# Kernel tuning notes

Measured on AMD Instinct MI355X. Metric: run time of the kernel, lower is better.

Reference implementation:

```python
import jax, jax.numpy as jnp
import numpy as np

D, H, DH, FF, L = 1024, 8, 128, 2048, 3
TEXT_V, UNIT_V = 128257, 10001
LN_EPS = 1e-5
TEMP = 0.0005
NEG = -1e9


def _layer_norm(x, s, b):
    m = x.mean(-1, keepdims=True)
    v = ((x - m) ** 2).mean(-1, keepdims=True)
    return (x - m) / jnp.sqrt(v + LN_EPS) * s + b


def _encoder(tokens, pad_idx, emb, ipw, ipb, ow, ob, l1s, l1b, f1w, f1b, f2w, f2b, l2s, l2b):
    pad = tokens == pad_idx  # [B,S] key padding mask
    x = emb[tokens]  # [B,S,D]; padding row of emb is zero
    B, S, _ = x.shape
    scale = 1.0 / np.sqrt(DH).astype(np.float32)
    for l in range(L):
        # --- self attention (post-norm, PyTorch TransformerEncoderLayer default) ---
        qkv = x @ ipw[l].T + ipb[l]  # [B,S,3D]
        q, k, v = jnp.split(qkv, 3, axis=-1)
        q = q.reshape(B, S, H, DH)
        k = k.reshape(B, S, H, DH)
        v = v.reshape(B, S, H, DH)
        scores = jnp.einsum('bqhd,bkhd->bhqk', q, k) * scale
        scores = jnp.where(pad[:, None, None, :], NEG, scores)
        attn = jax.nn.softmax(scores, axis=-1)
        o = jnp.einsum('bhqk,bkhd->bqhd', attn, v).reshape(B, S, D)
        o = o @ ow[l].T + ob[l]
        x = _layer_norm(x + o, l1s[l], l1b[l])
        # --- feedforward ---
        ff = jax.nn.relu(x @ f1w[l].T + f1b[l]) @ f2w[l].T + f2b[l]
        x = _layer_norm(x + ff, l2s[l], l2b[l])
    return x, pad


def _enc_params(key, V):
    ks = jax.random.split(key, 4)
    emb = jax.random.normal(ks[0], (V, D), jnp.float32) * 0.02
    emb = emb.at[V - 1].set(0.0)  # padding_idx row is zero
    return dict(
        emb=emb,
        ipw=jax.random.normal(ks[1], (L, 3 * D, D), jnp.float32) * 0.02,
        ipb=jnp.zeros((L, 3 * D), jnp.float32),
        ow=jax.random.normal(ks[2], (L, D, D), jnp.float32) * 0.02,
        ob=jnp.zeros((L, D), jnp.float32),
        l1s=jnp.ones((L, D), jnp.float32),
        l1b=jnp.zeros((L, D), jnp.float32),
        f1w=jax.random.normal(ks[3], (L, FF, D), jnp.float32) * 0.02,
        f1b=jnp.zeros((L, FF), jnp.float32),
        f2w=jax.random.normal(jax.random.fold_in(ks[3], 1), (L, D, FF), jnp.float32) * 0.02,
        f2b=jnp.zeros((L, D), jnp.float32),
        l2s=jnp.ones((L, D), jnp.float32),
        l2b=jnp.zeros((L, D), jnp.float32),
    )


def setup_inputs() -> dict:
    key = jax.random.key(0)
    k_tt, k_ut, k_tp, k_up = jax.random.split(key, 4)
    B, T, U = 8, 256, 1024
    inp = {
        'text_tokens': jax.random.randint(k_tt, (B, T), 0, TEXT_V - 1, jnp.int32),
        'unit_tokens': jax.random.randint(k_ut, (B, U), 0, UNIT_V - 1, jnp.int32),
    }
    for name, p in _enc_params(k_tp, TEXT_V).items():
        inp['t_' + name] = p
    for name, p in _enc_params(k_up, UNIT_V).items():
        inp['u_' + name] = p
    return inp


def reference(text_tokens, unit_tokens,
              t_emb, t_ipw, t_ipb, t_ow, t_ob, t_l1s, t_l1b, t_f1w, t_f1b, t_f2w, t_f2b, t_l2s, t_l2b,
              u_emb, u_ipw, u_ipb, u_ow, u_ob, u_l1s, u_l1b, u_f1w, u_f1b, u_f2w, u_f2b, u_l2s, u_l2b):
    tf, tpad = _encoder(text_tokens, TEXT_V - 1, t_emb, t_ipw, t_ipb, t_ow, t_ob,
                        t_l1s, t_l1b, t_f1w, t_f1b, t_f2w, t_f2b, t_l2s, t_l2b)
    uf, upad = _encoder(unit_tokens, UNIT_V - 1, u_emb, u_ipw, u_ipb, u_ow, u_ob,
                        u_l1s, u_l1b, u_f1w, u_f1b, u_f2w, u_f2b, u_l2s, u_l2b)
    # squared L2 distance via |a-b|^2 = |a|^2 + |b|^2 - 2 a.b (avoids [B,U,T,D] tensor)
    un = jnp.sum(uf * uf, axis=-1)  # [B,U]
    tn = jnp.sum(tf * tf, axis=-1)  # [B,T]
    cross = jnp.einsum('bud,btd->but', uf, tf)  # [B,U,T]
    dist = -TEMP * (un[:, :, None] + tn[:, None, :] - 2.0 * cross)
    mask = upad[:, :, None] | tpad[:, None, :]
    filled = jnp.where(mask, NEG, dist)
    return jax.nn.log_softmax(filled, axis=-1)  # [B,U,T]
```

## Files before the change

kernel.cpp:

```cpp
#include <hip/hip_runtime.h>
#include <stdint.h>

typedef _Float16 half_t;
typedef _Float16 half8 __attribute__((ext_vector_type(8)));
typedef float floatx4 __attribute__((ext_vector_type(4)));

#define D_MODEL 1024
#define NHEAD 8
#define DHEAD 128
#define FF_DIM 2048
#define NLAYER 3
#define BATCH 8
#define TSEQ 256
#define USEQ 1024
#define TPAD 128256
#define UPAD 10000
#define TEMP_ 5e-4f
#define SCALE_QK 0.08838834764831845f

__device__ inline float blk_sum(float v, float* sh) {
#pragma unroll
  for (int o = 32; o; o >>= 1) v += __shfl_xor(v, o, 64);
  __syncthreads();
  if ((threadIdx.x & 63) == 0) sh[threadIdx.x >> 6] = v;
  __syncthreads();
  return sh[0] + sh[1] + sh[2] + sh[3];
}
__device__ inline float blk_max(float v, float* sh) {
#pragma unroll
  for (int o = 32; o; o >>= 1) v = fmaxf(v, __shfl_xor(v, o, 64));
  __syncthreads();
  if ((threadIdx.x & 63) == 0) sh[threadIdx.x >> 6] = v;
  __syncthreads();
  return fmaxf(fmaxf(sh[0], sh[1]), fmaxf(sh[2], sh[3]));
}

__global__ __launch_bounds__(256)
void gemm_bt_kernel(const half_t* __restrict__ A, long lda, long sAb, long sAz,
                    const half_t* __restrict__ B, long ldb, long sBb, long sBz,
                    float* __restrict__ Cf, half_t* __restrict__ Ch,
                    long ldc, long sCb, long sCz,
                    const float* __restrict__ bias,
                    int M, int N, int K, float alpha, int relu, int zdiv) {
  __shared__ __align__(16) half_t As[128 * 64];
  __shared__ __align__(16) half_t Bs[128 * 64];

  const int z = blockIdx.z;
  const int zb = z / zdiv, zh = z % zdiv;
  A += (long)zb * sAb + (long)zh * sAz;
  B += (long)zb * sBb + (long)zh * sBz;
  const long coff = (long)zb * sCb + (long)zh * sCz;

  const int tid = threadIdx.x;
  const int lane = tid & 63;
  const int wid = tid >> 6;
  const long row0 = (long)blockIdx.y * 128;
  const long col0 = (long)blockIdx.x * 128;

  const int srow = tid >> 3;
  const int sg = tid & 7;

  const int wm = (wid & 1) << 6;
  const int wn = (wid >> 1) << 6;
  const int fm = lane & 15;
  const int quad = lane >> 4;

  floatx4 acc[4][4] = {};

  for (int k0 = 0; k0 < K; k0 += 64) {
#pragma unroll
    for (int i = 0; i < 4; ++i) {
      const int r = srow + (i << 5);
      const int gsw = (sg ^ (r & 7)) << 3;
      uint4 va = *(const uint4*)(A + (row0 + r) * lda + k0 + (sg << 3));
      *(uint4*)(&As[(r << 6) + gsw]) = va;
      uint4 vb = *(const uint4*)(B + (col0 + r) * ldb + k0 + (sg << 3));
      *(uint4*)(&Bs[(r << 6) + gsw]) = vb;
    }
    __syncthreads();
#pragma unroll
    for (int kk = 0; kk < 64; kk += 32) {
      const int gq = (kk >> 3) + quad;
      half8 af[4], bfr[4];
#pragma unroll
      for (int mi = 0; mi < 4; ++mi) {
        const int r = wm + (mi << 4) + fm;
        af[mi] = *(const half8*)(&As[(r << 6) + ((gq ^ (r & 7)) << 3)]);
      }
#pragma unroll
      for (int ni = 0; ni < 4; ++ni) {
        const int r = wn + (ni << 4) + fm;
        bfr[ni] = *(const half8*)(&Bs[(r << 6) + ((gq ^ (r & 7)) << 3)]);
      }
#pragma unroll
      for (int mi = 0; mi < 4; ++mi)
#pragma unroll
        for (int ni = 0; ni < 4; ++ni)
          acc[mi][ni] = __builtin_amdgcn_mfma_f32_16x16x32_f16(af[mi], bfr[ni], acc[mi][ni], 0, 0, 0);
    }
    __syncthreads();
  }

#pragma unroll
  for (int ni = 0; ni < 4; ++ni) {
    const long col = col0 + wn + (ni << 4) + fm;
    const float bv = bias ? bias[col] : 0.0f;
#pragma unroll
    for (int mi = 0; mi < 4; ++mi) {
#pragma unroll
      for (int r = 0; r < 4; ++r) {
        const long row = row0 + wm + (mi << 4) + (quad << 2) + r;
        float v = acc[mi][ni][r] * alpha + bv;
        if (relu) v = fmaxf(v, 0.0f);
        const long idx = coff + row * ldc + col;
        if (Cf) Cf[idx] = v;
        if (Ch) Ch[idx] = (half_t)v;
      }
    }
  }
}

__global__ void cvt_kernel(const float* __restrict__ in, half_t* __restrict__ out, long n) {
  long i = (long)blockIdx.x * 256 + threadIdx.x;
  const long stride = (long)gridDim.x * 256;
  for (; i < n; i += stride) out[i] = (half_t)in[i];
}

__global__ __launch_bounds__(256) void embed_kernel(const int* __restrict__ tok,
                                                    const float* __restrict__ emb,
                                                    float* __restrict__ xf, half_t* __restrict__ xh) {
  const long r = blockIdx.x;
  const long src = (long)tok[r] * D_MODEL;
  for (int j = threadIdx.x; j < D_MODEL; j += 256) {
    const float v = emb[src + j];
    xf[r * D_MODEL + j] = v;
    xh[r * D_MODEL + j] = (half_t)v;
  }
}

__global__ __launch_bounds__(256) void ln_kernel(float* x, const float* y,
                                                 const float* s, const float* b, half_t* xh) {
  const int row = blockIdx.x, tid = threadIdx.x;
  float* xr = x + (long)row * D_MODEL;
  const float* yr = y + (long)row * D_MODEL;
  float v[4], sum = 0.f, sq = 0.f;
#pragma unroll
  for (int c = 0; c < 4; ++c) {
    const int j = tid + (c << 8);
    const float t = xr[j] + yr[j];
    v[c] = t; sum += t; sq += t * t;
  }
  __shared__ float sh[4];
  sum = blk_sum(sum, sh);
  sq = blk_sum(sq, sh);
  const float mean = sum * (1.0f / D_MODEL);
  const float var = sq * (1.0f / D_MODEL) - mean * mean;
  const float inv = rsqrtf(var + 1e-5f);
#pragma unroll
  for (int c = 0; c < 4; ++c) {
    const int j = tid + (c << 8);
    const float t = (v[c] - mean) * inv * s[j] + b[j];
    xr[j] = t;
    xh[(long)row * D_MODEL + j] = (half_t)t;
  }
}

__global__ __launch_bounds__(256) void softmax_kernel(half_t* sc, const int* __restrict__ tok,
                                                      int S, int padidx) {
  const int q = blockIdx.x, z = blockIdx.y;
  const int b = z >> 3;
  half_t* row = sc + (long)z * S * S + (long)q * S;
  const int* tb = tok + (long)b * S;
  const int nc = S >> 8;
  const int tid = threadIdx.x;
  float v[4];
  float m = -3e38f;
  for (int c = 0; c < nc; ++c) {
    const int j = tid + (c << 8);
    float x = (float)row[j];
    if (tb[j] == padidx) x = -1e9f;
    v[c] = x;
    m = fmaxf(m, x);
  }
  __shared__ float sh[4];
  m = blk_max(m, sh);
  float ssum = 0.f;
  for (int c = 0; c < nc; ++c) { v[c] = expf(v[c] - m); ssum += v[c]; }
  ssum = blk_sum(ssum, sh);
  const float inv = 1.0f / ssum;
  for (int c = 0; c < nc; ++c) row[tid + (c << 8)] = (half_t)(v[c] * inv);
}

__global__ __launch_bounds__(256) void vtrans_kernel(const half_t* __restrict__ qkv,
                                                     half_t* __restrict__ vt, int S) {
  __shared__ half_t tile[64][65];
  const int s0 = blockIdx.x * 64, d0 = blockIdx.y * 64, z = blockIdx.z;
  const int b = z >> 3, h = z & 7;
  const half_t* src = qkv + (long)b * S * (3 * D_MODEL) + 2 * D_MODEL + h * DHEAD;
  for (int idx = threadIdx.x; idx < 4096; idx += 256) {
    const int r = idx >> 6, c = idx & 63;
    tile[r][c] = src[(long)(s0 + r) * (3 * D_MODEL) + d0 + c];
  }
  __syncthreads();
  half_t* dst = vt + ((long)z * DHEAD + d0) * S + s0;
  for (int idx = threadIdx.x; idx < 4096; idx += 256) {
    const int r = idx >> 6, c = idx & 63;
    dst[(long)r * S + c] = tile[c][r];
  }
}

__global__ __launch_bounds__(256) void rowsq_kernel(const float* __restrict__ x, float* __restrict__ o) {
  const int row = blockIdx.x, tid = threadIdx.x;
  const float* xr = x + (long)row * D_MODEL;
  float s = 0.f;
#pragma unroll
  for (int c = 0; c < 4; ++c) { const float t = xr[tid + (c << 8)]; s += t * t; }
  __shared__ float sh[4];
  s = blk_sum(s, sh);
  if (tid == 0) o[row] = s;
}

__global__ __launch_bounds__(256) void dist_lsm_kernel(float* out, const float* __restrict__ un,
                                                       const float* __restrict__ tn,
                                                       const int* __restrict__ utok,
                                                       const int* __restrict__ ttok) {
  const int u = blockIdx.x, b = blockIdx.y, t = threadIdx.x;
  const long off = ((long)(b * USEQ + u)) * TSEQ;
  const float c = out[off + t];
  float x = -TEMP_ * (un[b * USEQ + u] + tn[b * TSEQ + t] - 2.0f * c);
  if (utok[b * USEQ + u] == UPAD || ttok[b * TSEQ + t] == TPAD) x = -1e9f;
  __shared__ float sh[4];
  const float m = blk_max(x, sh);
  const float e = expf(x - m);
  const float s = blk_sum(e, sh);
  out[off + t] = x - m - logf(s);
}

static void launch_gemm(hipStream_t st, const half_t* A, long lda, long sAb, long sAz,
                        const half_t* B, long ldb, long sBb, long sBz,
                        float* Cf, half_t* Ch, long ldc, long sCb, long sCz,
                        const float* bias, int M, int N, int K, float alpha, int relu,
                        int zdiv, int nz) {
  dim3 g(N / 128, M / 128, nz), blk(256);
  gemm_bt_kernel<<<g, blk, 0, st>>>(A, lda, sAb, sAz, B, ldb, sBb, sBz,
                                    Cf, Ch, ldc, sCb, sCz, bias, M, N, K, alpha, relu, zdiv);
}

struct EncW {
  const int* tok; int S;
  const float *emb, *ipb, *ob, *l1s, *l1b, *f1b, *f2b, *l2s, *l2b;
  const half_t *ipw, *ow, *f1w, *f2w;
  int padidx;
};
struct Bufs {
  float *xf, *yf;
  half_t *xh, *qkv, *vt, *sc, *oh, *ffh;
};

static void run_encoder(hipStream_t st, const EncW& w, const Bufs& bb) {
  const int S = w.S, Ntok = BATCH * S;
  embed_kernel<<<Ntok, 256, 0, st>>>(w.tok, w.emb, bb.xf, bb.xh);
  for (int l = 0; l < NLAYER; ++l) {
    launch_gemm(st, bb.xh, D_MODEL, 0, 0,
                w.ipw + (size_t)l * 3 * D_MODEL * D_MODEL, D_MODEL, 0, 0,
                nullptr, bb.qkv, 3 * D_MODEL, 0, 0,
                w.ipb + (size_t)l * 3 * D_MODEL, Ntok, 3 * D_MODEL, D_MODEL, 1.0f, 0, 1, 1);
    vtrans_kernel<<<dim3(S / 64, DHEAD / 64, BATCH * NHEAD), 256, 0, st>>>(bb.qkv, bb.vt, S);
    launch_gemm(st, bb.qkv, 3 * D_MODEL, (long)S * 3 * D_MODEL, DHEAD,
                bb.qkv + D_MODEL, 3 * D_MODEL, (long)S * 3 * D_MODEL, DHEAD,
                nullptr, bb.sc, S, (long)NHEAD * S * S, (long)S * S,
                nullptr, S, S, DHEAD, SCALE_QK, 0, NHEAD, BATCH * NHEAD);
    softmax_kernel<<<dim3(S, BATCH * NHEAD), 256, 0, st>>>(bb.sc, w.tok, S, w.padidx);
    launch_gemm(st, bb.sc, S, (long)NHEAD * S * S, (long)S * S,
                bb.vt, S, (long)NHEAD * DHEAD * S, (long)DHEAD * S,
                nullptr, bb.oh, D_MODEL, (long)S * D_MODEL, DHEAD,
                nullptr, S, DHEAD, S, 1.0f, 0, NHEAD, BATCH * NHEAD);
    launch_gemm(st, bb.oh, D_MODEL, 0, 0,
                w.ow + (size_t)l * D_MODEL * D_MODEL, D_MODEL, 0, 0,
                bb.yf, nullptr, D_MODEL, 0, 0,
                w.ob + (size_t)l * D_MODEL, Ntok, D_MODEL, D_MODEL, 1.0f, 0, 1, 1);
    ln_kernel<<<Ntok, 256, 0, st>>>(bb.xf, bb.yf, w.l1s + (size_t)l * D_MODEL,
                                    w.l1b + (size_t)l * D_MODEL, bb.xh);
    launch_gemm(st, bb.xh, D_MODEL, 0, 0,
                w.f1w + (size_t)l * FF_DIM * D_MODEL, D_MODEL, 0, 0,
                nullptr, bb.ffh, FF_DIM, 0, 0,
                w.f1b + (size_t)l * FF_DIM, Ntok, FF_DIM, D_MODEL, 1.0f, 1, 1, 1);
    launch_gemm(st, bb.ffh, FF_DIM, 0, 0,
                w.f2w + (size_t)l * D_MODEL * FF_DIM, FF_DIM, 0, 0,
                bb.yf, nullptr, D_MODEL, 0, 0,
                w.f2b + (size_t)l * D_MODEL, Ntok, D_MODEL, FF_DIM, 1.0f, 0, 1, 1);
    ln_kernel<<<Ntok, 256, 0, st>>>(bb.xf, bb.yf, w.l2s + (size_t)l * D_MODEL,
                                    w.l2b + (size_t)l * D_MODEL, bb.xh);
  }
}

extern "C" void kernel_launch(void* const* d_in, const int* in_sizes, int n_in,
                              void* d_out, int out_size, void* d_ws, size_t ws_size,
                              hipStream_t stream) {
  (void)in_sizes; (void)n_in; (void)out_size; (void)ws_size;
  const int* ttok = (const int*)d_in[0];
  const int* utok = (const int*)d_in[1];
  const float* tp[13];
  const float* up[13];
  for (int i = 0; i < 13; ++i) tp[i] = (const float*)d_in[2 + i];
  for (int i = 0; i < 13; ++i) up[i] = (const float*)d_in[15 + i];

  char* wp = (char*)d_ws;
  auto alloc = [&](size_t bytes) {
    void* p = wp;
    wp += (bytes + 255) & ~(size_t)255;
    return p;
  };
  const size_t IPW = (size_t)NLAYER * 3 * D_MODEL * D_MODEL;
  const size_t OW = (size_t)NLAYER * D_MODEL * D_MODEL;
  const size_t F1W = (size_t)NLAYER * FF_DIM * D_MODEL;
  const size_t F2W = (size_t)NLAYER * D_MODEL * FF_DIM;
  half_t* t_ipw = (half_t*)alloc(IPW * 2);
  half_t* t_ow = (half_t*)alloc(OW * 2);
  half_t* t_f1w = (half_t*)alloc(F1W * 2);
  half_t* t_f2w = (half_t*)alloc(F2W * 2);
  half_t* u_ipw = (half_t*)alloc(IPW * 2);
  half_t* u_ow = (half_t*)alloc(OW * 2);
  half_t* u_f1w = (half_t*)alloc(F1W * 2);
  half_t* u_f2w = (half_t*)alloc(F2W * 2);
  Bufs bb;
  bb.xf = (float*)alloc((size_t)BATCH * USEQ * D_MODEL * 4);
  bb.yf = (float*)alloc((size_t)BATCH * USEQ * D_MODEL * 4);
  bb.xh = (half_t*)alloc((size_t)BATCH * USEQ * D_MODEL * 2);
  bb.qkv = (half_t*)alloc((size_t)BATCH * USEQ * 3 * D_MODEL * 2);
  bb.vt = (half_t*)alloc((size_t)BATCH * NHEAD * DHEAD * USEQ * 2);
  bb.sc = (half_t*)alloc((size_t)BATCH * NHEAD * USEQ * USEQ * 2);
  bb.oh = (half_t*)alloc((size_t)BATCH * USEQ * D_MODEL * 2);
  bb.ffh = (half_t*)alloc((size_t)BATCH * USEQ * FF_DIM * 2);
  half_t* tfh = (half_t*)alloc((size_t)BATCH * TSEQ * D_MODEL * 2);
  float* tn = (float*)alloc((size_t)BATCH * TSEQ * 4);
  float* un = (float*)alloc((size_t)BATCH * USEQ * 4);

  cvt_kernel<<<2048, 256, 0, stream>>>(tp[1], t_ipw, (long)IPW);
  cvt_kernel<<<2048, 256, 0, stream>>>(tp[3], t_ow, (long)OW);
  cvt_kernel<<<2048, 256, 0, stream>>>(tp[7], t_f1w, (long)F1W);
  cvt_kernel<<<2048, 256, 0, stream>>>(tp[9], t_f2w, (long)F2W);
  cvt_kernel<<<2048, 256, 0, stream>>>(up[1], u_ipw, (long)IPW);
  cvt_kernel<<<2048, 256, 0, stream>>>(up[3], u_ow, (long)OW);
  cvt_kernel<<<2048, 256, 0, stream>>>(up[7], u_f1w, (long)F1W);
  cvt_kernel<<<2048, 256, 0, stream>>>(up[9], u_f2w, (long)F2W);

  EncW tw{ttok, TSEQ, tp[0], tp[2], tp[4], tp[5], tp[6], tp[8], tp[10], tp[11], tp[12],
          t_ipw, t_ow, t_f1w, t_f2w, TPAD};
  run_encoder(stream, tw, bb);
  rowsq_kernel<<<BATCH * TSEQ, 256, 0, stream>>>(bb.xf, tn);
  hipMemcpyAsync(tfh, bb.xh, (size_t)BATCH * TSEQ * D_MODEL * 2, hipMemcpyDeviceToDevice, stream);

  EncW uw{utok, USEQ, up[0], up[2], up[4], up[5], up[6], up[8], up[10], up[11], up[12],
          u_ipw, u_ow, u_f1w, u_f2w, UPAD};
  run_encoder(stream, uw, bb);
  rowsq_kernel<<<BATCH * USEQ, 256, 0, stream>>>(bb.xf, un);

  float* out = (float*)d_out;
  launch_gemm(stream, bb.xh, D_MODEL, (long)USEQ * D_MODEL, 0,
              tfh, D_MODEL, (long)TSEQ * D_MODEL, 0,
              out, nullptr, TSEQ, (long)USEQ * TSEQ, 0,
              nullptr, USEQ, TSEQ, D_MODEL, 1.0f, 0, 1, BATCH);
  dist_lsm_kernel<<<dim3(USEQ, BATCH), 256, 0, stream>>>(out, un, tn, utok, ttok);
}
```

Before: 2.931 ms.

## Use direct global-to-LDS loads in GEMM and vectorize elementwise kernels

The GEMM tile loads now use the global_load_lds builtin, so data goes straight from global memory into shared memory without a round-trip through registers. The swizzle moves from the LDS destination to the global source address. Separately, the cvt, embed, layernorm, rowsq and softmax kernels switch to float4/half4 vectorized accesses, and the cvt grid size is halved. This cuts register pressure and memory instruction count, at the risk that the new lane-to-LDS mapping does not match what the fragment reads expect.

Result: faster. 2.748 ms (-6.2%).

```diff
diff --git a/kernel.cpp b/kernel.cpp
--- a/kernel.cpp
+++ b/kernel.cpp
@@ -2,6 +2,7 @@
 #include <stdint.h>
 
 typedef _Float16 half_t;
+typedef _Float16 half4 __attribute__((ext_vector_type(4)));
 typedef _Float16 half8 __attribute__((ext_vector_type(8)));
 typedef float floatx4 __attribute__((ext_vector_type(4)));
 
@@ -35,6 +36,12 @@
   return fmaxf(fmaxf(sh[0], sh[1]), fmaxf(sh[2], sh[3]));
 }
 
+typedef const __attribute__((address_space(1))) uint32_t* gas1_u32;
+typedef __attribute__((address_space(3))) uint32_t* las3_u32;
+__device__ __forceinline__ void gload16(const half_t* g, half_t* l) {
+  __builtin_amdgcn_global_load_lds((gas1_u32)g, (las3_u32)l, 16, 0, 0);
+}
+
 __global__ __launch_bounds__(256)
 void gemm_bt_kernel(const half_t* __restrict__ A, long lda, long sAb, long sAz,
                     const half_t* __restrict__ B, long ldb, long sBb, long sBz,
@@ -57,8 +64,8 @@
   const long row0 = (long)blockIdx.y * 128;
   const long col0 = (long)blockIdx.x * 128;
 
-  const int srow = tid >> 3;
-  const int sg = tid & 7;
+  const int srw = lane >> 3;
+  const int sg = lane & 7;
 
   const int wm = (wid & 1) << 6;
   const int wn = (wid >> 1) << 6;
@@ -70,12 +77,11 @@
   for (int k0 = 0; k0 < K; k0 += 64) {
 #pragma unroll
     for (int i = 0; i < 4; ++i) {
-      const int r = srow + (i << 5);
-      const int gsw = (sg ^ (r & 7)) << 3;
-      uint4 va = *(const uint4*)(A + (row0 + r) * lda + k0 + (sg << 3));
-      *(uint4*)(&As[(r << 6) + gsw]) = va;
-      uint4 vb = *(const uint4*)(B + (col0 + r) * ldb + k0 + (sg << 3));
-      *(uint4*)(&Bs[(r << 6) + gsw]) = vb;
+      const int rb = (i << 5) + (wid << 3);
+      const int rr = rb + srw;
+      const int gg = sg ^ (rr & 7);
+      gload16(A + (row0 + rr) * lda + k0 + (gg << 3), &As[rb << 6]);
+      gload16(B + (col0 + rr) * ldb + k0 + (gg << 3), &Bs[rb << 6]);
     }
     __syncthreads();
 #pragma unroll
@@ -121,9 +127,15 @@
 }
 
 __global__ void cvt_kernel(const float* __restrict__ in, half_t* __restrict__ out, long n) {
+  const long n4 = n >> 2;
   long i = (long)blockIdx.x * 256 + threadIdx.x;
   const long stride = (long)gridDim.x * 256;
-  for (; i < n; i += stride) out[i] = (half_t)in[i];
+  for (; i < n4; i += stride) {
+    const float4 v = *(const float4*)(in + (i << 2));
+    half4 h;
+    h[0] = (half_t)v.x; h[1] = (half_t)v.y; h[2] = (half_t)v.z; h[3] = (half_t)v.w;
+    *(half4*)(out + (i << 2)) = h;
+  }
 }
 
 __global__ __launch_bounds__(256) void embed_kernel(const int* __restrict__ tok,
@@ -131,38 +143,42 @@
                                                     float* __restrict__ xf, half_t* __restrict__ xh) {
   const long r = blockIdx.x;
   const long src = (long)tok[r] * D_MODEL;
-  for (int j = threadIdx.x; j < D_MODEL; j += 256) {
-    const float v = emb[src + j];
-    xf[r * D_MODEL + j] = v;
-    xh[r * D_MODEL + j] = (half_t)v;
-  }
+  const int j = threadIdx.x << 2;
+  const float4 v = *(const float4*)(emb + src + j);
+  *(float4*)(xf + r * D_MODEL + j) = v;
+  half4 h;
+  h[0] = (half_t)v.x; h[1] = (half_t)v.y; h[2] = (half_t)v.z; h[3] = (half_t)v.w;
+  *(half4*)(xh + r * D_MODEL + j) = h;
 }
 
 __global__ __launch_bounds__(256) void ln_kernel(float* x, const float* y,
                                                  const float* s, const float* b, half_t* xh) {
   const int row = blockIdx.x, tid = threadIdx.x;
+  const int j0 = tid << 2;
   float* xr = x + (long)row * D_MODEL;
   const float* yr = y + (long)row * D_MODEL;
-  float v[4], sum = 0.f, sq = 0.f;
-#pragma unroll
-  for (int c = 0; c < 4; ++c) {
-    const int j = tid + (c << 8);
-    const float t = xr[j] + yr[j];
-    v[c] = t; sum += t; sq += t * t;
-  }
+  const float4 xv = *(const float4*)(xr + j0);
+  const float4 yv = *(const float4*)(yr + j0);
+  float v[4] = {xv.x + yv.x, xv.y + yv.y, xv.z + yv.z, xv.w + yv.w};
+  float sum = v[0] + v[1] + v[2] + v[3];
+  float sq = v[0] * v[0] + v[1] * v[1] + v[2] * v[2] + v[3] * v[3];
   __shared__ float sh[4];
   sum = blk_sum(sum, sh);
   sq = blk_sum(sq, sh);
   const float mean = sum * (1.0f / D_MODEL);
   const float var = sq * (1.0f / D_MODEL) - mean * mean;
   const float inv = rsqrtf(var + 1e-5f);
-#pragma unroll
-  for (int c = 0; c < 4; ++c) {
-    const int j = tid + (c << 8);
-    const float t = (v[c] - mean) * inv * s[j] + b[j];
-    xr[j] = t;
-    xh[(long)row * D_MODEL + j] = (half_t)t;
-  }
+  const float4 sv = *(const float4*)(s + j0);
+  const float4 bv = *(const float4*)(b + j0);
+  float4 ov;
+  ov.x = (v[0] - mean) * inv * sv.x + bv.x;
+  ov.y = (v[1] - mean) * inv * sv.y + bv.y;
+  ov.z = (v[2] - mean) * inv * sv.z + bv.z;
+  ov.w = (v[3] - mean) * inv * sv.w + bv.w;
+  *(float4*)(xr + j0) = ov;
+  half4 h;
+  h[0] = (half_t)ov.x; h[1] = (half_t)ov.y; h[2] = (half_t)ov.z; h[3] = (half_t)ov.w;
+  *(half4*)(xh + (long)row * D_MODEL + j0) = h;
 }
 
 __global__ __launch_bounds__(256) void softmax_kernel(half_t* sc, const int* __restrict__ tok,
@@ -171,24 +187,36 @@
   const int b = z >> 3;
   half_t* row = sc + (long)z * S * S + (long)q * S;
   const int* tb = tok + (long)b * S;
-  const int nc = S >> 8;
   const int tid = threadIdx.x;
-  float v[4];
-  float m = -3e38f;
-  for (int c = 0; c < nc; ++c) {
-    const int j = tid + (c << 8);
-    float x = (float)row[j];
-    if (tb[j] == padidx) x = -1e9f;
-    v[c] = x;
-    m = fmaxf(m, x);
-  }
   __shared__ float sh[4];
-  m = blk_max(m, sh);
-  float ssum = 0.f;
-  for (int c = 0; c < nc; ++c) { v[c] = expf(v[c] - m); ssum += v[c]; }
-  ssum = blk_sum(ssum, sh);
-  const float inv = 1.0f / ssum;
-  for (int c = 0; c < nc; ++c) row[tid + (c << 8)] = (half_t)(v[c] * inv);
+  if (S == 1024) {
+    const int j0 = tid << 2;
+    const half4 h = *(const half4*)(row + j0);
+    const int4 tk = *(const int4*)(tb + j0);
+    float v[4];
+    v[0] = (tk.x == padidx) ? -1e9f : (float)h[0];
+    v[1] = (tk.y == padidx) ? -1e9f : (float)h[1];
+    v[2] = (tk.z == padidx) ? -1e9f : (float)h[2];
+    v[3] = (tk.w == padidx) ? -1e9f : (float)h[3];
+    float m = fmaxf(fmaxf(v[0], v[1]), fmaxf(v[2], v[3]));
+    m = blk_max(m, sh);
+    float ssum = 0.f;
+#pragma unroll
+    for (int c = 0; c < 4; ++c) { v[c] = expf(v[c] - m); ssum += v[c]; }
+    ssum = blk_sum(ssum, sh);
+    const float inv = 1.0f / ssum;
+    half4 o;
+#pragma unroll
+    for (int c = 0; c < 4; ++c) o[c] = (half_t)(v[c] * inv);
+    *(half4*)(row + j0) = o;
+  } else {
+    float x = (float)row[tid];
+    if (tb[tid] == padidx) x = -1e9f;
+    const float m = blk_max(x, sh);
+    const float e = expf(x - m);
+    const float ssum = blk_sum(e, sh);
+    row[tid] = (half_t)(e / ssum);
+  }
 }
 
 __global__ __launch_bounds__(256) void vtrans_kernel(const half_t* __restrict__ qkv,
@@ -212,9 +240,8 @@
 __global__ __launch_bounds__(256) void rowsq_kernel(const float* __restrict__ x, float* __restrict__ o) {
   const int row = blockIdx.x, tid = threadIdx.x;
   const float* xr = x + (long)row * D_MODEL;
-  float s = 0.f;
-#pragma unroll
-  for (int c = 0; c < 4; ++c) { const float t = xr[tid + (c << 8)]; s += t * t; }
+  const float4 v = *(const float4*)(xr + (tid << 2));
+  float s = v.x * v.x + v.y * v.y + v.z * v.z + v.w * v.w;
   __shared__ float sh[4];
   s = blk_sum(s, sh);
   if (tid == 0) o[row] = s;
@@ -336,14 +363,14 @@
   float* tn = (float*)alloc((size_t)BATCH * TSEQ * 4);
   float* un = (float*)alloc((size_t)BATCH * USEQ * 4);
 
-  cvt_kernel<<<2048, 256, 0, stream>>>(tp[1], t_ipw, (long)IPW);
-  cvt_kernel<<<2048, 256, 0, stream>>>(tp[3], t_ow, (long)OW);
-  cvt_kernel<<<2048, 256, 0, stream>>>(tp[7], t_f1w, (long)F1W);
-  cvt_kernel<<<2048, 256, 0, stream>>>(tp[9], t_f2w, (long)F2W);
-  cvt_kernel<<<2048, 256, 0, stream>>>(up[1], u_ipw, (long)IPW);
-  cvt_kernel<<<2048, 256, 0, stream>>>(up[3], u_ow, (long)OW);
-  cvt_kernel<<<2048, 256, 0, stream>>>(up[7], u_f1w, (long)F1W);
-  cvt_kernel<<<2048, 256, 0, stream>>>(up[9], u_f2w, (long)F2W);
+  cvt_kernel<<<1024, 256, 0, stream>>>(tp[1], t_ipw, (long)IPW);
+  cvt_kernel<<<1024, 256, 0, stream>>>(tp[3], t_ow, (long)OW);
+  cvt_kernel<<<1024, 256, 0, stream>>>(tp[7], t_f1w, (long)F1W);
+  cvt_kernel<<<1024, 256, 0, stream>>>(tp[9], t_f2w, (long)F2W);
+  cvt_kernel<<<1024, 256, 0, stream>>>(up[1], u_ipw, (long)IPW);
+  cvt_kernel<<<1024, 256, 0, stream>>>(up[3], u_ow, (long)OW);
+  cvt_kernel<<<1024, 256, 0, stream>>>(up[7], u_f1w, (long)F1W);
+  cvt_kernel<<<1024, 256, 0, stream>>>(up[9], u_f2w, (long)F2W);
 
   EncW tw{ttok, TSEQ, tp[0], tp[2], tp[4], tp[5], tp[6], tp[8], tp[10], tp[11], tp[12],
           t_ipw, t_ow, t_f1w, t_f2w, TPAD};
```
